# Kernel optimization log

Measured on AMD Instinct MI355X. Metric: run time of the kernel, lower is better.

Reference implementation:

```python
import jax, jax.numpy as jnp
import numpy as np


def setup_inputs() -> dict:
    key = jax.random.key(0)
    k1, k2 = jax.random.split(key)
    N, resolution = 32, 512
    cam2world_matrix = jax.random.normal(k1, (N, 4, 4), dtype=jnp.float32)
    # keep fx, fy (divisors) away from zero
    intrinsics = jax.random.uniform(k2, (N, 3, 3), dtype=jnp.float32, minval=0.5, maxval=1.5)
    return {"cam2world_matrix": cam2world_matrix, "intrinsics": intrinsics, "resolution": resolution}


def reference(cam2world_matrix, intrinsics, resolution):
    # patch_scale=1, masked_sampling=0 default path: full_resolution == resolution
    N = cam2world_matrix.shape[0]
    M = resolution * resolution
    cam_locs_world = cam2world_matrix[:, :3, 3]              # (N, 3)
    fx = intrinsics[:, 0, 0][:, None]
    fy = intrinsics[:, 1, 1][:, None]
    cx = intrinsics[:, 0, 2][:, None]
    cy = intrinsics[:, 1, 2][:, None]
    sk = intrinsics[:, 0, 1][:, None]

    # pixel-center uv grid in [0,1); torch builds (i,j) then flips channels,
    # so x_cam is the flattened column (j) grid, y_cam the row (i) grid.
    coords = (jnp.arange(resolution, dtype=jnp.float32) + 0.5) / resolution
    ii, jj = jnp.meshgrid(coords, coords, indexing='ij')      # (R, R) each
    x_cam = jj.reshape(1, M)                                  # broadcast over N
    y_cam = ii.reshape(1, M)
    z_cam = -1.0                                              # z_cam = -ones

    x_lift = -(x_cam - cx + cy * sk / fy - sk * y_cam / fy) / fx * z_cam  # (N, M)
    y_lift = (y_cam - cy) / fy * z_cam                                    # (N, M)

    ones = jnp.ones((N, M), dtype=cam2world_matrix.dtype)
    cam_rel_points = jnp.stack(
        (jnp.broadcast_to(x_lift, (N, M)),
         jnp.broadcast_to(y_lift, (N, M)),
         -ones, ones), axis=-1)                               # (N, M, 4)

    world_rel_points = jnp.einsum('nij,nmj->nmi', cam2world_matrix, cam_rel_points)[:, :, :3]
    ray_dirs = world_rel_points - cam_locs_world[:, None, :]
    norm = jnp.maximum(jnp.linalg.norm(ray_dirs, axis=2, keepdims=True), 1e-12)
    ray_dirs = ray_dirs / norm
    ray_origins = jnp.broadcast_to(cam_locs_world[:, None, :], ray_dirs.shape)
    return ray_origins, ray_dirs
```

## Files before the change

kernel.cpp:

```cpp
#include <hip/hip_runtime.h>
#include <math.h>

typedef float f32x4 __attribute__((ext_vector_type(4)));

__global__ __launch_bounds__(256) void ray_sampler_contig(
    const float* __restrict__ c2w,
    const float* __restrict__ intr,
    float* __restrict__ out,
    int blocks_per_cam,
    int resShift,
    float inv_res,
    size_t dir_off)
{
    const unsigned n   = (unsigned)blockIdx.x / (unsigned)blocks_per_cam;
    const unsigned blk = (unsigned)blockIdx.x - n * (unsigned)blocks_per_cam;
    const unsigned q   = blk * 256u + threadIdx.x;
    const unsigned f4_per_cam = (unsigned)blocks_per_cam * 256u;

    const float* C = c2w + n * 16;
    const float* K = intr + n * 9;

    const float r00 = C[0], r01 = C[1], r02 = C[2], ox = C[3];
    const float r10 = C[4], r11 = C[5], r12 = C[6], oy = C[7];
    const float r20 = C[8], r21 = C[9], r22 = C[10], oz = C[11];
    const float fx = K[0], sk = K[1], cx = K[2];
    const float fy = K[4], cy = K[5];

    const float inv_fx = 1.0f / fx;
    const float inv_fy = 1.0f / fy;

    const unsigned f0    = q * 4u;
    const unsigned p0    = f0 / 3u;
    const unsigned phase = f0 - p0 * 3u;
    const unsigned rmask = (1u << resShift) - 1u;

    const size_t t = (size_t)n * f4_per_cam + q;

    {
        const float ax = (phase == 0u) ? ox : ((phase == 1u) ? oy : oz);
        const float ay = (phase == 0u) ? oy : ((phase == 1u) ? oz : ox);
        const float az = (phase == 0u) ? oz : ((phase == 1u) ? ox : oy);
        const f32x4 vo = {ax, ay, az, ax};
        __builtin_nontemporal_store(vo, reinterpret_cast<f32x4*>(out) + t);
    }

    float d0x, d0y, d0z, d1x, d1y, d1z;
    #pragma unroll
    for (int s = 0; s < 2; ++s) {
        const unsigned p = p0 + (unsigned)s;
        const unsigned i = p >> resShift;
        const unsigned j = p & rmask;

        const float y_cam  = ((float)i + 0.5f) * inv_res;
        const float ycc    = (y_cam - cy) * inv_fy;
        const float y_lift = -ycc;
        const float xc_off = -cx - sk * ycc;
        const float x_cam  = ((float)j + 0.5f) * inv_res;
        const float x_lift = (x_cam + xc_off) * inv_fx;

        const float ux = fmaf(r00, x_lift, fmaf(r01, y_lift, -r02));
        const float uy = fmaf(r10, x_lift, fmaf(r11, y_lift, -r12));
        const float uz = fmaf(r20, x_lift, fmaf(r21, y_lift, -r22));
        const float ss  = fmaf(ux, ux, fmaf(uy, uy, uz * uz));
        const float inv = rsqrtf(fmaxf(ss, 1e-24f));

        if (s == 0) { d0x = ux * inv; d0y = uy * inv; d0z = uz * inv; }
        else        { d1x = ux * inv; d1y = uy * inv; d1z = uz * inv; }
    }

    f32x4 vd;
    vd.x = (phase == 0u) ? d0x : ((phase == 1u) ? d0y : d0z);
    vd.y = (phase == 0u) ? d0y : ((phase == 1u) ? d0z : d1x);
    vd.z = (phase == 0u) ? d0z : ((phase == 1u) ? d1x : d1y);
    vd.w = (phase == 0u) ? d1x : ((phase == 1u) ? d1y : d1z);
    __builtin_nontemporal_store(vd, reinterpret_cast<f32x4*>(out + dir_off) + t);
}

extern "C" void kernel_launch(void* const* d_in, const int* in_sizes, int n_in,
                              void* d_out, int out_size, void* d_ws, size_t ws_size,
                              hipStream_t stream) {
    const float* c2w  = (const float*)d_in[0];
    const float* intr = (const float*)d_in[1];
    float* out = (float*)d_out;

    const int N = in_sizes[0] / 16;
    const long long M = (long long)out_size / (6LL * (long long)N);
    const int res = (int)(sqrt((double)M) + 0.5);

    int resShift = 0; while ((1 << resShift) < res) ++resShift;

    const long long F    = (long long)N * M * 3LL;
    const int f4_per_cam = (int)(M * 3LL / 4LL);
    const int blocks_per_cam = f4_per_cam / 256;
    const int grid = N * blocks_per_cam;
    const size_t dir_off = (size_t)F;

    ray_sampler_contig<<<grid, 256, 0, stream>>>(c2w, intr, out,
                                                 blocks_per_cam, resShift,
                                                 1.0f / (float)res, dir_off);
}
```

Measured before the change: 204.2 us.

## Process eight float4 chunks per thread and use regular stores

Each thread now writes eight strided float4 chunks for both origins and directions, so the grid is eight times smaller. The aim is to amortize block scheduling and the per-camera parameter loads, and to keep more stores in flight per thread. Nontemporal store hints are replaced by ordinary stores, which changes how the writes interact with the cache. The risk is fewer waves to hide latency, and it relies on f4_per_cam being divisible by 2048.

```diff
diff --git a/kernel.cpp b/kernel.cpp
--- a/kernel.cpp
+++ b/kernel.cpp
@@ -3,7 +3,7 @@
 
 typedef float f32x4 __attribute__((ext_vector_type(4)));
 
-__global__ __launch_bounds__(256) void ray_sampler_contig(
+__global__ __launch_bounds__(256) void ray_sampler_deep(
     const float* __restrict__ c2w,
     const float* __restrict__ intr,
     float* __restrict__ out,
@@ -14,8 +14,7 @@
 {
     const unsigned n   = (unsigned)blockIdx.x / (unsigned)blocks_per_cam;
     const unsigned blk = (unsigned)blockIdx.x - n * (unsigned)blocks_per_cam;
-    const unsigned q   = blk * 256u + threadIdx.x;
-    const unsigned f4_per_cam = (unsigned)blocks_per_cam * 256u;
+    const unsigned f4_per_cam = (unsigned)blocks_per_cam * 2048u;
 
     const float* C = c2w + n * 16;
     const float* K = intr + n * 9;
@@ -28,52 +27,64 @@
 
     const float inv_fx = 1.0f / fx;
     const float inv_fy = 1.0f / fy;
-
-    const unsigned f0    = q * 4u;
-    const unsigned p0    = f0 / 3u;
-    const unsigned phase = f0 - p0 * 3u;
     const unsigned rmask = (1u << resShift) - 1u;
 
-    const size_t t = (size_t)n * f4_per_cam + q;
+    const unsigned q0  = blk * 2048u + threadIdx.x;
+    const unsigned f00 = q0 * 4u;
+    const size_t   t0  = (size_t)n * f4_per_cam + q0;
 
-    {
-        const float ax = (phase == 0u) ? ox : ((phase == 1u) ? oy : oz);
-        const float ay = (phase == 0u) ? oy : ((phase == 1u) ? oz : ox);
-        const float az = (phase == 0u) ? oz : ((phase == 1u) ? ox : oy);
+    f32x4* o4 = reinterpret_cast<f32x4*>(out);
+    f32x4* d4 = reinterpret_cast<f32x4*>(out + dir_off);
+
+    #pragma unroll
+    for (int k = 0; k < 8; ++k) {
+        const unsigned f0 = f00 + 1024u * (unsigned)k;
+        const unsigned p0 = f0 / 3u;
+        const unsigned ph = f0 - p0 * 3u;
+        const float ax = (ph == 0u) ? ox : ((ph == 1u) ? oy : oz);
+        const float ay = (ph == 0u) ? oy : ((ph == 1u) ? oz : ox);
+        const float az = (ph == 0u) ? oz : ((ph == 1u) ? ox : oy);
         const f32x4 vo = {ax, ay, az, ax};
-        __builtin_nontemporal_store(vo, reinterpret_cast<f32x4*>(out) + t);
+        o4[t0 + 256u * (unsigned)k] = vo;
     }
 
-    float d0x, d0y, d0z, d1x, d1y, d1z;
     #pragma unroll
-    for (int s = 0; s < 2; ++s) {
-        const unsigned p = p0 + (unsigned)s;
-        const unsigned i = p >> resShift;
-        const unsigned j = p & rmask;
+    for (int k = 0; k < 8; ++k) {
+        const unsigned f0 = f00 + 1024u * (unsigned)k;
+        const unsigned p0 = f0 / 3u;
+        const unsigned ph = f0 - p0 * 3u;
 
-        const float y_cam  = ((float)i + 0.5f) * inv_res;
-        const float ycc    = (y_cam - cy) * inv_fy;
-        const float y_lift = -ycc;
-        const float xc_off = -cx - sk * ycc;
-        const float x_cam  = ((float)j + 0.5f) * inv_res;
-        const float x_lift = (x_cam + xc_off) * inv_fx;
+        float d0x, d0y, d0z, d1x, d1y, d1z;
+        #pragma unroll
+        for (int s = 0; s < 2; ++s) {
+            const unsigned p = p0 + (unsigned)s;
+            const unsigned i = p >> resShift;
+            const unsigned j = p & rmask;
 
-        const float ux = fmaf(r00, x_lift, fmaf(r01, y_lift, -r02));
-        const float uy = fmaf(r10, x_lift, fmaf(r11, y_lift, -r12));
-        const float uz = fmaf(r20, x_lift, fmaf(r21, y_lift, -r22));
-        const float ss  = fmaf(ux, ux, fmaf(uy, uy, uz * uz));
-        const float inv = rsqrtf(fmaxf(ss, 1e-24f));
+            const float y_cam  = ((float)i + 0.5f) * inv_res;
+            const float ycc    = (y_cam - cy) * inv_fy;
+            const float y_lift = -ycc;
+            const float xc_off = -cx - sk * ycc;
+            const float x_cam  = ((float)j + 0.5f) * inv_res;
+            const float x_lift = (x_cam + xc_off) * inv_fx;
 
-        if (s == 0) { d0x = ux * inv; d0y = uy * inv; d0z = uz * inv; }
-        else        { d1x = ux * inv; d1y = uy * inv; d1z = uz * inv; }
+            const float ux = fmaf(r00, x_lift, fmaf(r01, y_lift, -r02));
+            const float uy = fmaf(r10, x_lift, fmaf(r11, y_lift, -r12));
+            const float uz = fmaf(r20, x_lift, fmaf(r21, y_lift, -r22));
+            const float ss  = fmaf(ux, ux, fmaf(uy, uy, uz * uz));
+            const float inv = rsqrtf(fmaxf(ss, 1e-24f));
+
+            if (s == 0) { d0x = ux * inv; d0y = uy * inv; d0z = uz * inv; }
+            else        { d1x = ux * inv; d1y = uy * inv; d1z = uz * inv; }
+        }
+
+        f32x4 vd;
+        vd.x = (ph == 0u) ? d0x : ((ph == 1u) ? d0y : d0z);
+        vd.y = (ph == 0u) ? d0y : ((ph == 1u) ? d0z : d1x);
+        vd.z = (ph == 0u) ? d0z : ((ph == 1u) ? d1x : d1y);
+        vd.w = (ph == 0u) ? d1x : ((ph == 1u) ? d1y : d1z);
+        d4[t0 + 256u * (unsigned)k] = vd;
     }
-
-    f32x4 vd;
-    vd.x = (phase == 0u) ? d0x : ((phase == 1u) ? d0y : d0z);
-    vd.y = (phase == 0u) ? d0y : ((phase == 1u) ? d0z : d1x);
-    vd.z = (phase == 0u) ? d0z : ((phase == 1u) ? d1x : d1y);
-    vd.w = (phase == 0u) ? d1x : ((phase == 1u) ? d1y : d1z);
-    __builtin_nontemporal_store(vd, reinterpret_cast<f32x4*>(out + dir_off) + t);
 }
 
 extern "C" void kernel_launch(void* const* d_in, const int* in_sizes, int n_in,
@@ -91,11 +102,11 @@
 
     const long long F    = (long long)N * M * 3LL;
     const int f4_per_cam = (int)(M * 3LL / 4LL);
-    const int blocks_per_cam = f4_per_cam / 256;
+    const int blocks_per_cam = f4_per_cam / 2048;
     const int grid = N * blocks_per_cam;
     const size_t dir_off = (size_t)F;
 
-    ray_sampler_contig<<<grid, 256, 0, stream>>>(c2w, intr, out,
-                                                 blocks_per_cam, resShift,
-                                                 1.0f / (float)res, dir_off);
+    ray_sampler_deep<<<grid, 256, 0, stream>>>(c2w, intr, out,
+                                               blocks_per_cam, resShift,
+                                               1.0f / (float)res, dir_off);
 }
```

Result: faster. 196.1 us (-4.0%).
